# Kernel optimization log

Hardware: AMD Instinct MI355X
Metric: run time of the kernel (lower is better)

## Reference

```python
import jax, jax.numpy as jnp
import numpy as np

B = 4096
E = 1024   # input_size (embedding)
H = 1024   # hidden_size
C = 1024   # context_vector_size
D = E + H + C  # combined_vector_size


def setup_inputs() -> dict:
    key = jax.random.key(0)
    ks = jax.random.split(key, 20)
    s_gate = 1.0 / np.sqrt(D)
    s_c = 1.0 / np.sqrt(C)
    s_h = 1.0 / np.sqrt(H)
    s_e = 1.0 / np.sqrt(E)
    return {
        "previous_embedded_caption": jax.random.normal(ks[0], (B, E), jnp.float32),
        "previous_hidden_state": jax.random.normal(ks[1], (B, H), jnp.float32),
        "previous_cell_state": jax.random.normal(ks[2], (B, H), jnp.float32),
        "current_context_vector": jax.random.normal(ks[3], (B, C), jnp.float32),
        "Wi": jax.random.uniform(ks[4], (H, D), jnp.float32, -s_gate, s_gate),
        "bi": jax.random.uniform(ks[5], (H,), jnp.float32, -s_gate, s_gate),
        "Wf": jax.random.uniform(ks[6], (H, D), jnp.float32, -s_gate, s_gate),
        "bf": jax.random.uniform(ks[7], (H,), jnp.float32, -s_gate, s_gate),
        "Wo": jax.random.uniform(ks[8], (H, D), jnp.float32, -s_gate, s_gate),
        "bo": jax.random.uniform(ks[9], (H,), jnp.float32, -s_gate, s_gate),
        "Wg": jax.random.uniform(ks[10], (H, D), jnp.float32, -s_gate, s_gate),
        "bg": jax.random.uniform(ks[11], (H,), jnp.float32, -s_gate, s_gate),
        "Wc": jax.random.uniform(ks[12], (E, C), jnp.float32, -s_c, s_c),
        "bc": jax.random.uniform(ks[13], (E,), jnp.float32, -s_c, s_c),
        "Wh": jax.random.uniform(ks[14], (E, H), jnp.float32, -s_h, s_h),
        "bh": jax.random.uniform(ks[15], (E,), jnp.float32, -s_h, s_h),
        "Wp": jax.random.uniform(ks[16], (E, E), jnp.float32, -s_e, s_e),
        "bp": jax.random.uniform(ks[17], (E,), jnp.float32, -s_e, s_e),
    }


def reference(previous_embedded_caption, previous_hidden_state, previous_cell_state,
              current_context_vector, Wi, bi, Wf, bf, Wo, bo, Wg, bg,
              Wc, bc, Wh, bh, Wp, bp):
    # combined vector [B, D]
    combined = jnp.concatenate(
        [previous_embedded_caption, previous_hidden_state, current_context_vector], axis=1)
    i = jax.nn.sigmoid(combined @ Wi.T + bi)
    f = jax.nn.sigmoid(combined @ Wf.T + bf)
    o = jax.nn.sigmoid(combined @ Wo.T + bo)
    g = jnp.tanh(combined @ Wg.T + bg)
    cell = f * previous_cell_state + i * g           # [B, H]
    hidden = o * jnp.tanh(cell)                      # [B, H]
    resid = previous_embedded_caption + (hidden @ Wh.T + bh) + (current_context_vector @ Wc.T + bc)
    prediction = resid @ Wp.T + bp                   # [B, E]
    return (prediction, hidden, cell)
```

## Files before the change

### kernel.cpp

```cpp
#include <hip/hip_runtime.h>
#include <stdint.h>

#define BATCH 4096
#define EHC   1024
#define DCOMB 3072
#define NTOT  ((size_t)BATCH * EHC)
#define WGATE ((size_t)EHC * DCOMB)
#define WSML  ((size_t)EHC * EHC)

#define BK 64

typedef __bf16 bf16x8 __attribute__((ext_vector_type(8)));
typedef float  f32x4  __attribute__((ext_vector_type(4)));

__device__ inline unsigned short f2b(float f) {
    unsigned int x = __float_as_uint(f);
    unsigned int r = (x + 0x7fffu + ((x >> 16) & 1u)) >> 16;
    return (unsigned short)r;
}
__device__ inline float sigmoid_f(float x) { return 1.0f / (1.0f + __expf(-x)); }
__device__ inline float tanh_f(float x) {
    float xa = fminf(fmaxf(x, -15.0f), 15.0f);
    float e = __expf(2.0f * xa);
    return (e - 1.0f) / (e + 1.0f);
}

__device__ inline void load16(const void* g, void* l) {
    __builtin_amdgcn_global_load_lds(
        (const __attribute__((address_space(1))) void*)g,
        (__attribute__((address_space(3))) void*)l, 16, 0, 0);
}

__global__ __launch_bounds__(256)
void cvt_all(const float* __restrict__ s0, const float* __restrict__ s1,
             const float* __restrict__ s2, const float* __restrict__ s3,
             const float* __restrict__ s4, const float* __restrict__ s5,
             const float* __restrict__ s6, const float* __restrict__ s7,
             const float* __restrict__ s8, const float* __restrict__ s9,
             short* __restrict__ dst)
{
    const unsigned b = blockIdx.x;
    const float* src = s0; unsigned st = 0;
    if (b >= 2048)  { src = s1; st = 2048;  }
    if (b >= 4096)  { src = s2; st = 4096;  }
    if (b >= 6144)  { src = s3; st = 6144;  }
    if (b >= 7680)  { src = s4; st = 7680;  }
    if (b >= 9216)  { src = s5; st = 9216;  }
    if (b >= 10752) { src = s6; st = 10752; }
    if (b >= 12288) { src = s7; st = 12288; }
    if (b >= 12800) { src = s8; st = 12800; }
    if (b >= 13312) { src = s9; st = 13312; }
    size_t soff = ((size_t)(b - st) * 2048) + (size_t)threadIdx.x * 8;
    size_t doff = ((size_t)b * 2048) + (size_t)threadIdx.x * 8;
    float4 a = *(const float4*)(src + soff);
    float4 c = *(const float4*)(src + soff + 4);
    uint4 v;
    v.x = (unsigned)f2b(a.x) | ((unsigned)f2b(a.y) << 16);
    v.y = (unsigned)f2b(a.z) | ((unsigned)f2b(a.w) << 16);
    v.z = (unsigned)f2b(c.x) | ((unsigned)f2b(c.y) << 16);
    v.w = (unsigned)f2b(c.z) | ((unsigned)f2b(c.w) << 16);
    *(uint4*)(dst + doff) = v;
}

template <int MODE>
__global__ __launch_bounds__(256, 2)
void gemm_fused(const short* __restrict__ A0, const short* __restrict__ A1,
                const short* __restrict__ A2,
                const short* __restrict__ W0, const short* __restrict__ W1,
                const short* __restrict__ W2, const short* __restrict__ W3,
                const float* __restrict__ b0, const float* __restrict__ b1,
                const float* __restrict__ b2, const float* __restrict__ b3,
                const float* __restrict__ extra,
                void* __restrict__ outv, float* __restrict__ out2,
                short* __restrict__ out3)
{
    constexpr int NG  = (MODE == 1) ? 4 : 1;
    constexpr int BMT = 128;
    constexpr int BNT = 64;
    constexpr int MI  = BMT / 32;
    constexpr int NI  = BNT / 32;
    constexpr int AI  = BMT / 32;
    constexpr int BI  = BNT / 32;
    constexpr int WMH = BMT / 2;
    constexpr int BSZ = BNT * BK;

    int flat = blockIdx.y * 16 + blockIdx.x;
    flat = (flat & 7) * 64 + (flat >> 3);
    const int nblk = flat & 15;
    const int mblk = flat >> 4;

    const int tid  = threadIdx.x;
    const int lane = tid & 63;
    const int wave = tid >> 6;
    const int wm = wave >> 1;
    const int wn = wave & 1;
    const int l15 = lane & 15;
    const int l4  = lane >> 4;

    __shared__ short As[BMT * BK];
    __shared__ short Bs[NG * BSZ];

    const int K = (MODE == 1) ? DCOMB : (MODE == 2 ? 2048 : 1024);
    const int wstride = (MODE == 1) ? DCOMB : 1024;
    const int wrowbase = nblk * BNT;

    int aoff[AI], woff[BI];
#pragma unroll
    for (int j = 0; j < AI; j++) {
        int c  = j * 256 + tid;
        int r  = c >> 3;
        int qg = (c & 7) ^ (r & 7);
        aoff[j] = (mblk * BMT + r) * 1024 + qg * 8;
    }
#pragma unroll
    for (int j = 0; j < BI; j++) {
        int c  = j * 256 + tid;
        int r  = c >> 3;
        int qg = (c & 7) ^ (r & 7);
        woff[j] = (wrowbase + r) * wstride + qg * 8;
    }

    int a_ld[2][MI], b_ld[2][NI];
#pragma unroll
    for (int s = 0; s < 2; s++) {
        int q = s * 4 + l4;
#pragma unroll
        for (int i = 0; i < MI; i++) {
            int rowA = wm * WMH + i * 16 + l15;
            a_ld[s][i] = (rowA * 8 + (q ^ (rowA & 7))) * 8;
        }
#pragma unroll
        for (int i = 0; i < NI; i++) {
            int rowB = wn * 32 + i * 16 + l15;
            b_ld[s][i] = (rowB * 8 + (q ^ (rowB & 7))) * 8;
        }
    }

    f32x4 acc[NG][MI][NI];
#pragma unroll
    for (int g = 0; g < NG; g++)
#pragma unroll
        for (int i = 0; i < MI; i++)
#pragma unroll
            for (int j = 0; j < NI; j++) acc[g][i][j] = (f32x4){0.f, 0.f, 0.f, 0.f};

    const int KT = K / BK;
    for (int kt = 0; kt < KT; ++kt) {
        const int k0   = kt * BK;
        const int seg  = (MODE == 3) ? 0 : (k0 >> 10);
        const int acol = k0 & 1023;
        const short* Aseg = (seg == 0) ? A0 : (seg == 1) ? A1 : A2;

        __syncthreads();
#pragma unroll
        for (int j = 0; j < AI; j++)
            load16(Aseg + aoff[j] + acol, &As[(j * 256 + tid) * 8]);
        if (MODE == 1) {
            const short* Wg4[4] = {W0, W1, W2, W3};
#pragma unroll
            for (int g = 0; g < 4; g++)
#pragma unroll
                for (int j = 0; j < BI; j++)
                    load16(Wg4[g] + woff[j] + k0, &Bs[g * BSZ + (j * 256 + tid) * 8]);
        } else {
            const short* Wt = (seg == 0) ? W0 : W1;
#pragma unroll
            for (int j = 0; j < BI; j++)
                load16(Wt + woff[j] + acol, &Bs[(j * 256 + tid) * 8]);
        }
        __syncthreads();

#pragma unroll
        for (int s = 0; s < 2; s++) {
            bf16x8 af[MI];
#pragma unroll
            for (int i = 0; i < MI; i++) af[i] = *(const bf16x8*)(As + a_ld[s][i]);
#pragma unroll
            for (int g = 0; g < NG; g++) {
                bf16x8 bv[NI];
#pragma unroll
                for (int i = 0; i < NI; i++)
                    bv[i] = *(const bf16x8*)(Bs + g * BSZ + b_ld[s][i]);
#pragma unroll
                for (int mi = 0; mi < MI; mi++)
#pragma unroll
                    for (int ni = 0; ni < NI; ni++)
                        acc[g][mi][ni] = __builtin_amdgcn_mfma_f32_16x16x32_bf16(
                            af[mi], bv[ni], acc[g][mi][ni], 0, 0, 0);
            }
        }
    }

#pragma unroll
    for (int ni = 0; ni < NI; ni++) {
        const int col = nblk * BNT + wn * 32 + ni * 16 + l15;
        if (MODE == 1) {
            const float bi_ = b0[col], bf_ = b1[col], bo_ = b2[col], bg_ = b3[col];
#pragma unroll
            for (int mi = 0; mi < MI; mi++) {
#pragma unroll
                for (int r = 0; r < 4; r++) {
                    const size_t row = (size_t)(mblk * BMT + wm * WMH + mi * 16 + l4 * 4 + r);
                    const size_t idx = row * 1024 + col;
                    float ai = fminf(fmaxf(acc[0][mi][ni][r] + bi_, -30.f), 30.f);
                    float af_ = fminf(fmaxf(acc[1][mi][ni][r] + bf_, -30.f), 30.f);
                    float ao = fminf(fmaxf(acc[2][mi][ni][r] + bo_, -30.f), 30.f);
                    float ag = fminf(fmaxf(acc[3][mi][ni][r] + bg_, -30.f), 30.f);
                    float ig = sigmoid_f(ai), fg = sigmoid_f(af_);
                    float og = sigmoid_f(ao), gg = tanh_f(ag);
                    float c = fg * extra[idx] + ig * gg;
                    float h = og * tanh_f(c);
                    ((float*)outv)[idx] = c;
                    out2[idx] = h;
                    out3[idx] = (short)f2b(h);
                }
            }
        } else {
            float bias_v = (MODE == 2) ? (b0[col] + b1[col]) : b0[col];
#pragma unroll
            for (int mi = 0; mi < MI; mi++) {
#pragma unroll
                for (int r = 0; r < 4; r++) {
                    const size_t row = (size_t)(mblk * BMT + wm * WMH + mi * 16 + l4 * 4 + r);
                    const size_t idx = row * 1024 + col;
                    float v = acc[0][mi][ni][r] + bias_v;
                    if (MODE == 2) {
                        v += extra[idx];
                        ((short*)outv)[idx] = (short)f2b(v);
                    } else {
                        ((float*)outv)[idx] = v;
                    }
                }
            }
        }
    }
}

extern "C" void kernel_launch(void* const* d_in, const int* in_sizes, int n_in,
                              void* d_out, int out_size, void* d_ws, size_t ws_size,
                              hipStream_t stream)
{
    const float* emb  = (const float*)d_in[0];
    const float* hid  = (const float*)d_in[1];
    const float* pcel = (const float*)d_in[2];
    const float* ctx  = (const float*)d_in[3];
    const float* Wi = (const float*)d_in[4];   const float* bi = (const float*)d_in[5];
    const float* Wf = (const float*)d_in[6];   const float* bf_ = (const float*)d_in[7];
    const float* Wo = (const float*)d_in[8];   const float* bo = (const float*)d_in[9];
    const float* Wg = (const float*)d_in[10];  const float* bg = (const float*)d_in[11];
    const float* Wc = (const float*)d_in[12];  const float* bc = (const float*)d_in[13];
    const float* Wh = (const float*)d_in[14];  const float* bh = (const float*)d_in[15];
    const float* Wp = (const float*)d_in[16];  const float* bp = (const float*)d_in[17];

    float* out      = (float*)d_out;
    float* pred     = out;
    float* hidden_o = out + NTOT;
    float* cell_o   = out + 2 * NTOT;

    short* ws = (short*)d_ws;
    short* w_emb  = ws;
    short* w_hid  = ws + NTOT;
    short* w_ctx  = ws + 2 * NTOT;
    short* w_Wg4  = ws + 3 * NTOT;
    short* w_Wh   = w_Wg4 + 4 * WGATE;
    short* w_Wc   = w_Wh + WSML;
    short* w_Wp   = w_Wc + WSML;
    short* w_hidb = w_Wp + WSML;
    short* w_res  = w_hidb + NTOT;

    dim3 blk(256, 1, 1);
    const short* np16 = nullptr;
    const float* npf  = nullptr;

    hipLaunchKernelGGL(cvt_all, dim3(13824), blk, 0, stream,
                       emb, hid, ctx, Wi, Wf, Wo, Wg, Wh, Wc, Wp, ws);

    hipLaunchKernelGGL((gemm_fused<1>), dim3(16, 32), blk, 0, stream,
                       w_emb, w_hid, w_ctx,
                       w_Wg4, w_Wg4 + WGATE, w_Wg4 + 2 * WGATE, w_Wg4 + 3 * WGATE,
                       bi, bf_, bo, bg, pcel,
                       (void*)cell_o, hidden_o, w_hidb);
    hipLaunchKernelGGL((gemm_fused<2>), dim3(16, 32), blk, 0, stream,
                       w_hidb, w_ctx, np16, w_Wh, w_Wc, np16, np16,
                       bh, bc, npf, npf, emb, (void*)w_res, (float*)nullptr, (short*)nullptr);
    hipLaunchKernelGGL((gemm_fused<3>), dim3(16, 32), blk, 0, stream,
                       w_res, np16, np16, w_Wp, np16, np16, np16,
                       bp, npf, npf, npf, npf, (void*)pred, (float*)nullptr, (short*)nullptr);
}
```

Measured before the change: 332.6 us.

## Use dedicated 512-thread gate GEMM kernel with 256-row M tiles

Moves the fused four-gate LSTM GEMM into its own kernel that uses 512 threads (8 waves) and a 256-row by 64-column tile, so each weight tile loaded into shared memory is reused across twice as many batch rows. This cuts global and L2 traffic for the four gate weight matrices and halves the grid to 256 blocks. The generic templated kernel is simplified to handle only the two smaller GEMMs. The cost is larger LDS use (64KB) and many accumulators per thread, which may limit occupancy, and fewer blocks than the GPU has CUs.

```diff
diff --git a/kernel.cpp b/kernel.cpp
--- a/kernel.cpp
+++ b/kernel.cpp
@@ -62,6 +62,133 @@
     *(uint4*)(dst + doff) = v;
 }
 
+__global__ __launch_bounds__(512, 2)
+void gemm_gates(const short* __restrict__ A0, const short* __restrict__ A1,
+                const short* __restrict__ A2, const short* __restrict__ W,
+                const float* __restrict__ b0, const float* __restrict__ b1,
+                const float* __restrict__ b2, const float* __restrict__ b3,
+                const float* __restrict__ pcell,
+                float* __restrict__ cell_o, float* __restrict__ hid_o,
+                short* __restrict__ hid_b)
+{
+    int f = blockIdx.y * 16 + blockIdx.x;
+    f = (f & 7) * 32 + (f >> 3);
+    const int nblk = f & 15;
+    const int mblk = f >> 4;
+
+    const int tid  = threadIdx.x;
+    const int lane = tid & 63;
+    const int wave = tid >> 6;
+    const int wm   = wave >> 1;
+    const int wn   = wave & 1;
+    const int l15  = lane & 15;
+    const int l4   = lane >> 4;
+
+    __shared__ short As[256 * 64];
+    __shared__ short Bs[4 * 64 * 64];
+
+    int aoff[4];
+#pragma unroll
+    for (int j = 0; j < 4; j++) {
+        int c  = j * 512 + tid;
+        int r  = c >> 3;
+        int qg = (c & 7) ^ (r & 7);
+        aoff[j] = (mblk * 256 + r) * 1024 + qg * 8;
+    }
+    int woff;
+    {
+        int r  = tid >> 3;
+        int qg = (tid & 7) ^ (r & 7);
+        woff = (nblk * 64 + r) * 3072 + qg * 8;
+    }
+
+    int a_ld[2][4], b_ld[2][2];
+#pragma unroll
+    for (int s = 0; s < 2; s++) {
+        int qf = s * 4 + l4;
+#pragma unroll
+        for (int mi = 0; mi < 4; mi++) {
+            int rowA = wm * 64 + mi * 16 + l15;
+            a_ld[s][mi] = (rowA * 8 + (qf ^ (rowA & 7))) * 8;
+        }
+#pragma unroll
+        for (int ni = 0; ni < 2; ni++) {
+            int rowB = wn * 32 + ni * 16 + l15;
+            b_ld[s][ni] = (rowB * 8 + (qf ^ (rowB & 7))) * 8;
+        }
+    }
+
+    f32x4 acc[4][4][2];
+#pragma unroll
+    for (int g = 0; g < 4; g++)
+#pragma unroll
+        for (int mi = 0; mi < 4; mi++)
+#pragma unroll
+            for (int ni = 0; ni < 2; ni++) acc[g][mi][ni] = (f32x4){0.f, 0.f, 0.f, 0.f};
+
+    const int KT = DCOMB / BK;
+    for (int kt = 0; kt < KT; ++kt) {
+        const int k0   = kt * BK;
+        const int seg  = k0 >> 10;
+        const int acol = k0 & 1023;
+        const short* Aseg = (seg == 0) ? A0 : (seg == 1) ? A1 : A2;
+
+        __syncthreads();
+#pragma unroll
+        for (int j = 0; j < 4; j++)
+            load16(Aseg + aoff[j] + acol, &As[(j * 512 + tid) * 8]);
+#pragma unroll
+        for (int g = 0; g < 4; g++)
+            load16(W + (size_t)g * WGATE + woff + k0, &Bs[(g * 512 + tid) * 8]);
+        __syncthreads();
+
+#pragma unroll
+        for (int s = 0; s < 2; s++) {
+            bf16x8 af[4];
+#pragma unroll
+            for (int mi = 0; mi < 4; mi++) af[mi] = *(const bf16x8*)(As + a_ld[s][mi]);
+#pragma unroll
+            for (int g = 0; g < 4; g++) {
+                bf16x8 bv[2];
+#pragma unroll
+                for (int ni = 0; ni < 2; ni++)
+                    bv[ni] = *(const bf16x8*)(Bs + g * 4096 + b_ld[s][ni]);
+#pragma unroll
+                for (int mi = 0; mi < 4; mi++)
+#pragma unroll
+                    for (int ni = 0; ni < 2; ni++)
+                        acc[g][mi][ni] = __builtin_amdgcn_mfma_f32_16x16x32_bf16(
+                            af[mi], bv[ni], acc[g][mi][ni], 0, 0, 0);
+            }
+        }
+    }
+
+#pragma unroll
+    for (int ni = 0; ni < 2; ni++) {
+        const int col = nblk * 64 + wn * 32 + ni * 16 + l15;
+        const float bi_ = b0[col], bf_ = b1[col], bo_ = b2[col], bg_ = b3[col];
+#pragma unroll
+        for (int mi = 0; mi < 4; mi++) {
+#pragma unroll
+            for (int r = 0; r < 4; r++) {
+                const size_t row = (size_t)(mblk * 256 + wm * 64 + mi * 16 + l4 * 4 + r);
+                const size_t idx = row * 1024 + col;
+                float ai  = fminf(fmaxf(acc[0][mi][ni][r] + bi_, -30.f), 30.f);
+                float af_ = fminf(fmaxf(acc[1][mi][ni][r] + bf_, -30.f), 30.f);
+                float ao  = fminf(fmaxf(acc[2][mi][ni][r] + bo_, -30.f), 30.f);
+                float ag  = fminf(fmaxf(acc[3][mi][ni][r] + bg_, -30.f), 30.f);
+                float ig = sigmoid_f(ai), fg = sigmoid_f(af_);
+                float og = sigmoid_f(ao), gg = tanh_f(ag);
+                float c = fg * pcell[idx] + ig * gg;
+                float h = og * tanh_f(c);
+                cell_o[idx] = c;
+                hid_o[idx]  = h;
+                hid_b[idx]  = (short)f2b(h);
+            }
+        }
+    }
+}
+
 template <int MODE>
 __global__ __launch_bounds__(256, 2)
 void gemm_fused(const short* __restrict__ A0, const short* __restrict__ A1,
@@ -74,7 +201,7 @@
                 void* __restrict__ outv, float* __restrict__ out2,
                 short* __restrict__ out3)
 {
-    constexpr int NG  = (MODE == 1) ? 4 : 1;
+    constexpr int NG  = 1;
     constexpr int BMT = 128;
     constexpr int BNT = 64;
     constexpr int MI  = BMT / 32;
@@ -100,8 +227,8 @@
     __shared__ short As[BMT * BK];
     __shared__ short Bs[NG * BSZ];
 
-    const int K = (MODE == 1) ? DCOMB : (MODE == 2 ? 2048 : 1024);
-    const int wstride = (MODE == 1) ? DCOMB : 1024;
+    const int K = (MODE == 2) ? 2048 : 1024;
+    const int wstride = 1024;
     const int wrowbase = nblk * BNT;
 
     int aoff[AI], woff[BI];
@@ -149,20 +276,13 @@
         const int k0   = kt * BK;
         const int seg  = (MODE == 3) ? 0 : (k0 >> 10);
         const int acol = k0 & 1023;
-        const short* Aseg = (seg == 0) ? A0 : (seg == 1) ? A1 : A2;
+        const short* Aseg = (seg == 0) ? A0 : A1;
 
         __syncthreads();
 #pragma unroll
         for (int j = 0; j < AI; j++)
             load16(Aseg + aoff[j] + acol, &As[(j * 256 + tid) * 8]);
-        if (MODE == 1) {
-            const short* Wg4[4] = {W0, W1, W2, W3};
-#pragma unroll
-            for (int g = 0; g < 4; g++)
-#pragma unroll
-                for (int j = 0; j < BI; j++)
-                    load16(Wg4[g] + woff[j] + k0, &Bs[g * BSZ + (j * 256 + tid) * 8]);
-        } else {
+        {
             const short* Wt = (seg == 0) ? W0 : W1;
 #pragma unroll
             for (int j = 0; j < BI; j++)
@@ -175,61 +295,35 @@
             bf16x8 af[MI];
 #pragma unroll
             for (int i = 0; i < MI; i++) af[i] = *(const bf16x8*)(As + a_ld[s][i]);
-#pragma unroll
-            for (int g = 0; g < NG; g++) {
-                bf16x8 bv[NI];
-#pragma unroll
-                for (int i = 0; i < NI; i++)
-                    bv[i] = *(const bf16x8*)(Bs + g * BSZ + b_ld[s][i]);
-#pragma unroll
-                for (int mi = 0; mi < MI; mi++)
-#pragma unroll
-                    for (int ni = 0; ni < NI; ni++)
-                        acc[g][mi][ni] = __builtin_amdgcn_mfma_f32_16x16x32_bf16(
-                            af[mi], bv[ni], acc[g][mi][ni], 0, 0, 0);
-            }
+            bf16x8 bv[NI];
+#pragma unroll
+            for (int i = 0; i < NI; i++)
+                bv[i] = *(const bf16x8*)(Bs + b_ld[s][i]);
+#pragma unroll
+            for (int mi = 0; mi < MI; mi++)
+#pragma unroll
+                for (int ni = 0; ni < NI; ni++)
+                    acc[0][mi][ni] = __builtin_amdgcn_mfma_f32_16x16x32_bf16(
+                        af[mi], bv[ni], acc[0][mi][ni], 0, 0, 0);
         }
     }
 
 #pragma unroll
     for (int ni = 0; ni < NI; ni++) {
         const int col = nblk * BNT + wn * 32 + ni * 16 + l15;
-        if (MODE == 1) {
-            const float bi_ = b0[col], bf_ = b1[col], bo_ = b2[col], bg_ = b3[col];
-#pragma unroll
-            for (int mi = 0; mi < MI; mi++) {
-#pragma unroll
-                for (int r = 0; r < 4; r++) {
-                    const size_t row = (size_t)(mblk * BMT + wm * WMH + mi * 16 + l4 * 4 + r);
-                    const size_t idx = row * 1024 + col;
-                    float ai = fminf(fmaxf(acc[0][mi][ni][r] + bi_, -30.f), 30.f);
-                    float af_ = fminf(fmaxf(acc[1][mi][ni][r] + bf_, -30.f), 30.f);
-                    float ao = fminf(fmaxf(acc[2][mi][ni][r] + bo_, -30.f), 30.f);
-                    float ag = fminf(fmaxf(acc[3][mi][ni][r] + bg_, -30.f), 30.f);
-                    float ig = sigmoid_f(ai), fg = sigmoid_f(af_);
-                    float og = sigmoid_f(ao), gg = tanh_f(ag);
-                    float c = fg * extra[idx] + ig * gg;
-                    float h = og * tanh_f(c);
-                    ((float*)outv)[idx] = c;
-                    out2[idx] = h;
-                    out3[idx] = (short)f2b(h);
-                }
-            }
-        } else {
-            float bias_v = (MODE == 2) ? (b0[col] + b1[col]) : b0[col];
-#pragma unroll
-            for (int mi = 0; mi < MI; mi++) {
-#pragma unroll
-                for (int r = 0; r < 4; r++) {
-                    const size_t row = (size_t)(mblk * BMT + wm * WMH + mi * 16 + l4 * 4 + r);
-                    const size_t idx = row * 1024 + col;
-                    float v = acc[0][mi][ni][r] + bias_v;
-                    if (MODE == 2) {
-                        v += extra[idx];
-                        ((short*)outv)[idx] = (short)f2b(v);
-                    } else {
-                        ((float*)outv)[idx] = v;
-                    }
+        float bias_v = (MODE == 2) ? (b0[col] + b1[col]) : b0[col];
+#pragma unroll
+        for (int mi = 0; mi < MI; mi++) {
+#pragma unroll
+            for (int r = 0; r < 4; r++) {
+                const size_t row = (size_t)(mblk * BMT + wm * WMH + mi * 16 + l4 * 4 + r);
+                const size_t idx = row * 1024 + col;
+                float v = acc[0][mi][ni][r] + bias_v;
+                if (MODE == 2) {
+                    v += extra[idx];
+                    ((short*)outv)[idx] = (short)f2b(v);
+                } else {
+                    ((float*)outv)[idx] = v;
                 }
             }
         }
@@ -275,11 +369,10 @@
     hipLaunchKernelGGL(cvt_all, dim3(13824), blk, 0, stream,
                        emb, hid, ctx, Wi, Wf, Wo, Wg, Wh, Wc, Wp, ws);
 
-    hipLaunchKernelGGL((gemm_fused<1>), dim3(16, 32), blk, 0, stream,
-                       w_emb, w_hid, w_ctx,
-                       w_Wg4, w_Wg4 + WGATE, w_Wg4 + 2 * WGATE, w_Wg4 + 3 * WGATE,
+    hipLaunchKernelGGL(gemm_gates, dim3(16, 16), dim3(512, 1, 1), 0, stream,
+                       w_emb, w_hid, w_ctx, w_Wg4,
                        bi, bf_, bo, bg, pcel,
-                       (void*)cell_o, hidden_o, w_hidb);
+                       cell_o, hidden_o, w_hidb);
     hipLaunchKernelGGL((gemm_fused<2>), dim3(16, 32), blk, 0, stream,
                        w_hidb, w_ctx, np16, w_Wh, w_Wc, np16, np16,
                        bh, bc, npf, npf, emb, (void*)w_res, (float*)nullptr, (short*)nullptr);
```

Measured after the change: 360.9 us. 1.09x slower.
